# Optimization experiments

Measured on AMD Instinct MI355X. Metric: run time of the kernel, lower is better.

Reference implementation:

```python
import jax, jax.numpy as jnp
import numpy as np

N = 100000   # num_nodes
E = 1250000  # num_edges
IN = 64
HID = 64
OUT = 64
LN_EPS = 1e-5


def _gcn_conv(x, src, dst, W, b, n):
    # PyG GCNConv: add self-loops, symmetric deg^{-1/2} normalization, then linear.
    h = x @ W  # (N, out)
    deg = jax.ops.segment_sum(jnp.ones(src.shape[0], h.dtype), dst, num_segments=n) + 1.0  # +1 self-loop
    dinv = jax.lax.rsqrt(deg)
    norm = dinv[src] * dinv[dst]  # (E,)
    out = jax.ops.segment_sum(h[src] * norm[:, None], dst, num_segments=n)
    out = out + h * (dinv * dinv)[:, None]  # self-loop message
    return out + b


def _sage_conv(x, src, dst, Wl, bl, Wr, n):
    # PyG SAGEConv(aggr='mean'): lin_l(mean_{j in N(i)} x_j) + lin_r(x_i); bias only in lin_l.
    cnt = jax.ops.segment_sum(jnp.ones(src.shape[0], x.dtype), dst, num_segments=n)
    agg = jax.ops.segment_sum(x[src], dst, num_segments=n) / jnp.maximum(cnt, 1.0)[:, None]
    return agg @ Wl + bl + x @ Wr


def _layer_norm(x, g, b):
    mu = jnp.mean(x, axis=-1, keepdims=True)
    var = jnp.var(x, axis=-1, keepdims=True)
    return (x - mu) * jax.lax.rsqrt(var + LN_EPS) * g + b


def setup_inputs() -> dict:
    key = jax.random.key(0)
    ks = jax.random.split(key, 16)
    def w(k, shape):
        fan_in = shape[0]
        return (jax.random.normal(k, shape, jnp.float32) / np.sqrt(fan_in)).astype(jnp.float32)
    x = jax.random.normal(ks[0], (N, IN), jnp.float32)
    edge_index = jax.random.randint(ks[1], (2, E), 0, N, dtype=jnp.int64)
    return {
        "x": x,
        "edge_index": edge_index,
        "gcn_w1": w(ks[2], (IN, HID)), "gcn_b1": jnp.zeros((HID,), jnp.float32),
        "gcn_w2": w(ks[3], (HID, OUT)), "gcn_b2": jnp.zeros((OUT,), jnp.float32),
        "sage_wl1": w(ks[4], (IN, HID)), "sage_bl1": jnp.zeros((HID,), jnp.float32),
        "sage_wr1": w(ks[5], (IN, HID)),
        "sage_wl2": w(ks[6], (HID, OUT)), "sage_bl2": jnp.zeros((OUT,), jnp.float32),
        "sage_wr2": w(ks[7], (HID, OUT)),
        "gcn_ln_g": jnp.ones((OUT,), jnp.float32), "gcn_ln_b": jnp.zeros((OUT,), jnp.float32),
        "sage_ln_g": jnp.ones((OUT,), jnp.float32), "sage_ln_b": jnp.zeros((OUT,), jnp.float32),
        "proj_w": w(ks[8], (2 * OUT, OUT)), "proj_b": jnp.zeros((OUT,), jnp.float32),
    }


def reference(x, edge_index, gcn_w1, gcn_b1, gcn_w2, gcn_b2,
              sage_wl1, sage_bl1, sage_wr1, sage_wl2, sage_bl2, sage_wr2,
              gcn_ln_g, gcn_ln_b, sage_ln_g, sage_ln_b, proj_w, proj_b):
    src, dst = edge_index[0], edge_index[1]
    n = x.shape[0]
    # GCN branch (dropout p=0 / eval -> identity)
    g = jax.nn.relu(_gcn_conv(x, src, dst, gcn_w1, gcn_b1, n))
    g = _gcn_conv(g, src, dst, gcn_w2, gcn_b2, n)
    # SAGE branch
    s = jax.nn.relu(_sage_conv(x, src, dst, sage_wl1, sage_bl1, sage_wr1, n))
    s = _sage_conv(s, src, dst, sage_wl2, sage_bl2, sage_wr2, n)
    # Norm + projected-concat fusion
    g = _layer_norm(g, gcn_ln_g, gcn_ln_b)
    s = _layer_norm(s, sage_ln_g, sage_ln_b)
    cat = jnp.concatenate([g, s], axis=-1)  # (N, 2*OUT)
    return cat @ proj_w + proj_b
```

## Files before the change

kernel.cpp:

```cpp
#include <hip/hip_runtime.h>


#define SCAN_CHUNK 2048

typedef __attribute__((ext_vector_type(8))) short short8;
typedef __attribute__((ext_vector_type(4))) short short4v;
typedef __attribute__((ext_vector_type(4))) float floatx4;

__device__ __forceinline__ unsigned short f2bf(float f) {
    unsigned int u = __float_as_uint(f);
    unsigned int r = u + 0x7FFFu + ((u >> 16) & 1u);
    return (unsigned short)(r >> 16);
}
__device__ __forceinline__ float bf2f(unsigned short h) {
    return __uint_as_float(((unsigned int)h) << 16);
}

__device__ __forceinline__ unsigned lds_addr(const void* p) {
    return (unsigned)(unsigned long long)(__attribute__((address_space(3))) const char*)p;
}

__device__ __forceinline__ short8 cat44(short4v lo, short4v hi) {
    short8 r;
    r[0] = lo[0]; r[1] = lo[1]; r[2] = lo[2]; r[3] = lo[3];
    r[4] = hi[0]; r[5] = hi[1]; r[6] = hi[2]; r[7] = hi[3];
    return r;
}

template<int NF, int CTB>
__device__ __forceinline__ void tr_read4(unsigned a0, short8 bf[4]) {
    short4v l0, h0, l1, h1, l2, h2, l3, h3;
    asm volatile(
        "ds_read_b64_tr_b16 %0, %8 offset:%9\n\t"
        "ds_read_b64_tr_b16 %1, %8 offset:%10\n\t"
        "ds_read_b64_tr_b16 %2, %8 offset:%11\n\t"
        "ds_read_b64_tr_b16 %3, %8 offset:%12\n\t"
        "ds_read_b64_tr_b16 %4, %8 offset:%13\n\t"
        "ds_read_b64_tr_b16 %5, %8 offset:%14\n\t"
        "ds_read_b64_tr_b16 %6, %8 offset:%15\n\t"
        "ds_read_b64_tr_b16 %7, %8 offset:%16\n\t"
        "s_waitcnt lgkmcnt(0)"
        : "=&v"(l0), "=&v"(h0), "=&v"(l1), "=&v"(h1),
          "=&v"(l2), "=&v"(h2), "=&v"(l3), "=&v"(h3)
        : "v"(a0),
          "i"((0 * NF + CTB + 0) * 128), "i"((1 * NF + CTB + 0) * 128),
          "i"((0 * NF + CTB + 1) * 128), "i"((1 * NF + CTB + 1) * 128),
          "i"((0 * NF + CTB + 2) * 128), "i"((1 * NF + CTB + 2) * 128),
          "i"((0 * NF + CTB + 3) * 128), "i"((1 * NF + CTB + 3) * 128)
        : "memory");
    bf[0] = cat44(l0, h0);
    bf[1] = cat44(l1, h1);
    bf[2] = cat44(l2, h2);
    bf[3] = cat44(l3, h3);
}

__global__ void k_count(const int* __restrict__ ei, int E, int* __restrict__ cnt,
                        int* __restrict__ rank,
                        const float* __restrict__ x, unsigned short* __restrict__ xb,
                        int xtotal, int do_x) {
    int i = blockIdx.x * blockDim.x + threadIdx.x;
    int e = i * 4;
    if (e + 4 <= E) {
        int4 d = *(const int4*)&ei[E + e];
        int4 r;
        r.x = atomicAdd(&cnt[d.x], 1);
        r.y = atomicAdd(&cnt[d.y], 1);
        r.z = atomicAdd(&cnt[d.z], 1);
        r.w = atomicAdd(&cnt[d.w], 1);
        *(int4*)&rank[e] = r;
    } else if (e < E) {
        for (int j = e; j < E; ++j) rank[j] = atomicAdd(&cnt[ei[E + j]], 1);
    }
    if (do_x) {
        int xe = i * 8;
        if (xe + 8 <= xtotal) {
            float4 a = *(const float4*)&x[xe];
            float4 b = *(const float4*)&x[xe + 4];
            short8 o;
            o[0] = (short)f2bf(a.x); o[1] = (short)f2bf(a.y);
            o[2] = (short)f2bf(a.z); o[3] = (short)f2bf(a.w);
            o[4] = (short)f2bf(b.x); o[5] = (short)f2bf(b.y);
            o[6] = (short)f2bf(b.z); o[7] = (short)f2bf(b.w);
            *(short8*)&xb[xe] = o;
        } else if (xe < xtotal) {
            for (int j = xe; j < xtotal; ++j) xb[j] = f2bf(x[j]);
        }
    }
}

__global__ void k_scan_reduce(const int* __restrict__ cnt, int N, int* __restrict__ blockSums) {
    __shared__ int lds[256];
    int base = blockIdx.x * SCAN_CHUNK;
    int t = threadIdx.x;
    int s = 0;
    for (int j = 0; j < 8; ++j) {
        int idx = base + t * 8 + j;
        if (idx < N) s += cnt[idx] + 1;
    }
    lds[t] = s;
    __syncthreads();
    for (int d = 128; d > 0; d >>= 1) {
        if (t < d) lds[t] += lds[t + d];
        __syncthreads();
    }
    if (t == 0) blockSums[blockIdx.x] = lds[0];
}

__global__ void k_scan_spine(int* __restrict__ blockSums, int B) {
    if (threadIdx.x == 0 && blockIdx.x == 0) {
        int run = 0;
        for (int b = 0; b < B; ++b) { int v = blockSums[b]; blockSums[b] = run; run += v; }
    }
}

__global__ void k_scan_write(const int* __restrict__ cnt, int N,
                             const int* __restrict__ blockSums,
                             int* __restrict__ offs, float* __restrict__ dinv) {
    __shared__ int lds[256];
    int base = blockIdx.x * SCAN_CHUNK;
    int t = threadIdx.x;
    int v[8];
    int s = 0;
    for (int j = 0; j < 8; ++j) {
        int idx = base + t * 8 + j;
        v[j] = (idx < N) ? cnt[idx] : 0;
        s += (idx < N) ? v[j] + 1 : 0;
    }
    lds[t] = s;
    __syncthreads();
    for (int d = 1; d < 256; d <<= 1) {
        int x = (t >= d) ? lds[t - d] : 0;
        __syncthreads();
        lds[t] += x;
        __syncthreads();
    }
    int excl = (t == 0) ? 0 : lds[t - 1];
    int run = blockSums[blockIdx.x] + excl;
    for (int j = 0; j < 8; ++j) {
        int idx = base + t * 8 + j;
        if (idx < N) {
            offs[idx] = run;
            run += v[j] + 1;
            dinv[idx] = rsqrtf((float)v[j] + 1.0f);
            if (idx == N - 1) offs[N] = run;
        }
    }
}

__global__ void k_fill(const int* __restrict__ ei, int E, const int* __restrict__ offs,
                       const int* __restrict__ rank, const int* __restrict__ cnt,
                       const float* __restrict__ dinv,
                       int* __restrict__ csr, unsigned int* __restrict__ pk,
                       int use_pk, int N) {
    int i = blockIdx.x * blockDim.x + threadIdx.x;
    int e = i * 4;
    if (e + 4 <= E) {
        int4 s = *(const int4*)&ei[e];
        int4 d = *(const int4*)&ei[E + e];
        int4 r = *(const int4*)&rank[e];
        int p0 = offs[d.x] + r.x, p1 = offs[d.y] + r.y;
        int p2 = offs[d.z] + r.z, p3 = offs[d.w] + r.w;
        csr[p0] = s.x; csr[p1] = s.y; csr[p2] = s.z; csr[p3] = s.w;
        if (use_pk) {
            pk[p0] = ((unsigned)(d.x & 15) << 16) | f2bf(dinv[s.x] * dinv[d.x]);
            pk[p1] = ((unsigned)(d.y & 15) << 16) | f2bf(dinv[s.y] * dinv[d.y]);
            pk[p2] = ((unsigned)(d.z & 15) << 16) | f2bf(dinv[s.z] * dinv[d.z]);
            pk[p3] = ((unsigned)(d.w & 15) << 16) | f2bf(dinv[s.w] * dinv[d.w]);
        }
    } else if (e < E) {
        for (int j = e; j < E; ++j) {
            int dd = ei[E + j];
            int p = offs[dd] + rank[j];
            csr[p] = ei[j];
            if (use_pk) pk[p] = ((unsigned)(dd & 15) << 16) | f2bf(dinv[ei[j]] * dinv[dd]);
        }
    }
    if (use_pk && i < N) {
        int pos = offs[i] + cnt[i];
        float di = dinv[i];
        csr[pos] = i;
        pk[pos] = ((unsigned)(i & 15) << 16) | (1u << 20) | f2bf(di * di);
    }
}

template<int ROWSH>
__launch_bounds__(256)
__global__ void k_gatherM(const unsigned short* __restrict__ feat,
                          const int* __restrict__ csr,
                          const unsigned int* __restrict__ pk,
                          const int* __restrict__ offs, const int* __restrict__ cnt,
                          unsigned short* __restrict__ agg, int N) {
    constexpr int NF = ROWSH / 16;
    constexpr int LPR = ROWSH / 8;
    constexpr int EPP = 64 / LPR;
    constexpr int PASSES = 32 / EPP;

    __shared__ unsigned short sbuf[4][32 * ROWSH];

    const int lane = threadIdx.x & 63;
    const int wv = threadIdx.x >> 6;
    const int base = blockIdx.x * 64 + wv * 16;
    if (base >= N) return;

    const int q = lane >> 4;
    const int d16 = lane & 15;

    const int parity = lane & 1;
    const int ei_low = (lane >> 1) & 3;
    const int sf_sub = (lane >> 3) & (NF - 1);
    const int ei_high = (NF == 8) ? 0 : (lane >> 5);
    const int eid = ei_high * 4 + ei_low;
    const int sf = sf_sub * 16 + parity * 8;

    const int elo = offs[base];
    const int ehi = offs[min(base + 16, N)];
    const int emax = ehi - 1;
    const int nch = (ehi - elo + 31) >> 5;

    int cM0, cM1, cM2, cM3;
    unsigned pM0, pM1, pM2, pM3;
    {
        int i0 = elo + lane;
        int i1 = i0 + 64, i2 = i0 + 128, i3 = i0 + 192;
        cM0 = csr[i0 <= emax ? i0 : emax];
        cM1 = csr[i1 <= emax ? i1 : emax];
        cM2 = csr[i2 <= emax ? i2 : emax];
        cM3 = csr[i3 <= emax ? i3 : emax];
        unsigned t0 = pk[i0 <= emax ? i0 : emax];
        unsigned t1 = pk[i1 <= emax ? i1 : emax];
        unsigned t2 = pk[i2 <= emax ? i2 : emax];
        unsigned t3 = pk[i3 <= emax ? i3 : emax];
        pM0 = (i0 < ehi) ? t0 : 0x00100000u;
        pM1 = (i1 < ehi) ? t1 : 0x00100000u;
        pM2 = (i2 < ehi) ? t2 : 0x00100000u;
        pM3 = (i3 < ehi) ? t3 : 0x00100000u;
    }

    floatx4 accg[4], accs[4];
#pragma unroll
    for (int i = 0; i < 4; ++i) {
        accg[i] = floatx4{0.f, 0.f, 0.f, 0.f};
        accs[i] = floatx4{0.f, 0.f, 0.f, 0.f};
    }

    unsigned short* wb = &sbuf[wv][0];
    const unsigned a0 = lds_addr(wb) + (unsigned)(q * 2 * NF) * 128u + (unsigned)d16 * 8u;

    for (int c = 0; c < nch; ++c) {
        int cv; unsigned pv; int wofs;
        int rc = c >> 1;
        if (rc < 4) {
            wofs = (c & 1) << 5;
            cv = (rc == 0) ? cM0 : (rc == 1) ? cM1 : (rc == 2) ? cM2 : cM3;
            pv = (rc == 0) ? pM0 : (rc == 1) ? pM1 : (rc == 2) ? pM2 : pM3;
        } else {
            int idx = elo + (c << 5) + lane;
            int idc = idx <= emax ? idx : emax;
            cv = csr[idc];
            unsigned t = pk[idc];
            pv = (idx < ehi) ? t : 0x00100000u;
            wofs = 0;
        }

        short8 stg[PASSES];
#pragma unroll
        for (int p = 0; p < PASSES; ++p) {
            int src = __shfl(cv, wofs + p * EPP + eid, 64);
            stg[p] = *(const short8*)&feat[(size_t)src * ROWSH + sf];
        }

        short8 aG, aS;
#pragma unroll
        for (int j = 0; j < 8; ++j) {
            unsigned u = (unsigned)__shfl((int)pv, wofs + q * 8 + j, 64);
            unsigned hi = u >> 16;
            bool match = (int)(hi & 15u) == d16;
            aG[j] = match ? (short)(u & 0xFFFFu) : (short)0;
            aS[j] = (match && !(hi & 16u)) ? (short)0x3F80 : (short)0;
        }

#pragma unroll
        for (int p = 0; p < PASSES; ++p)
            *(short8*)&wb[p * 512 + lane * 8] = stg[p];
        asm volatile("s_waitcnt lgkmcnt(0)" ::: "memory");
        __builtin_amdgcn_sched_barrier(0);

        short8 bG[4];
        tr_read4<NF, 0>(a0, bG);
#pragma unroll
        for (int ct = 0; ct < 4; ++ct)
            accg[ct] = __builtin_amdgcn_mfma_f32_16x16x32_bf16(aG, bG[ct], accg[ct], 0, 0, 0);
        if constexpr (NF == 8) {
            short8 bS[4];
            tr_read4<NF, 4>(a0, bS);
#pragma unroll
            for (int ct = 0; ct < 4; ++ct)
                accs[ct] = __builtin_amdgcn_mfma_f32_16x16x32_bf16(aS, bS[ct], accs[ct], 0, 0, 0);
        } else {
#pragma unroll
            for (int ct = 0; ct < 4; ++ct)
                accs[ct] = __builtin_amdgcn_mfma_f32_16x16x32_bf16(aS, bG[ct], accs[ct], 0, 0, 0);
        }
    }

#pragma unroll
    for (int r = 0; r < 4; ++r) {
        int node = base + q * 4 + r;
        if (node < N) {
            float rn = 1.0f / fmaxf((float)cnt[node], 1.0f);
#pragma unroll
            for (int ct = 0; ct < 4; ++ct) {
                agg[(size_t)node * 128 + ct * 16 + d16]      = f2bf(accg[ct][r]);
                agg[(size_t)node * 128 + 64 + ct * 16 + d16] = f2bf(accs[ct][r] * rn);
            }
        }
    }
}

__device__ __forceinline__ void xor_reduce8(float4& a, float4& b) {
    a.x += __shfl_xor(a.x, 16, 64); a.y += __shfl_xor(a.y, 16, 64);
    a.z += __shfl_xor(a.z, 16, 64); a.w += __shfl_xor(a.w, 16, 64);
    b.x += __shfl_xor(b.x, 16, 64); b.y += __shfl_xor(b.y, 16, 64);
    b.z += __shfl_xor(b.z, 16, 64); b.w += __shfl_xor(b.w, 16, 64);
    a.x += __shfl_xor(a.x, 32, 64); a.y += __shfl_xor(a.y, 32, 64);
    a.z += __shfl_xor(a.z, 32, 64); a.w += __shfl_xor(a.w, 32, 64);
    b.x += __shfl_xor(b.x, 32, 64); b.y += __shfl_xor(b.y, 32, 64);
    b.z += __shfl_xor(b.z, 32, 64); b.w += __shfl_xor(b.w, 32, 64);
}

__device__ __forceinline__ float red16(float v) {
    v += __shfl_xor(v, 1, 64);
    v += __shfl_xor(v, 2, 64);
    v += __shfl_xor(v, 4, 64);
    v += __shfl_xor(v, 8, 64);
    return v;
}

__global__ void k_gather1_f32(const float* __restrict__ x, const int* __restrict__ csr,
                              const int* __restrict__ offs, const int* __restrict__ cnt,
                              const float* __restrict__ dinv,
                              unsigned short* __restrict__ agg, int N) {
    int lane = threadIdx.x & 63;
    int wave = threadIdx.x >> 6;
    int node = blockIdx.x * 4 + wave;
    if (node >= N) return;
    int c = lane & 15, grp = lane >> 4;

    int st = offs[node];
    int cn = cnt[node];
    float di = dinv[node];

    float4 aA = {0.f, 0.f, 0.f, 0.f}, aB = {0.f, 0.f, 0.f, 0.f};
    for (int e = 0; e < cn; e += 8) {
        int i0 = e + grp, i1 = e + 4 + grp;
        float m0 = (i0 < cn) ? 1.f : 0.f;
        float m1 = (i1 < cn) ? 1.f : 0.f;
        int s0 = csr[st + (i0 < cn ? i0 : cn - 1)];
        int s1 = csr[st + (i1 < cn ? i1 : cn - 1)];
        float w0 = m0 * dinv[s0];
        float w1 = m1 * dinv[s1];
        float4 v0 = *(const float4*)&x[(size_t)s0 * 64 + 4 * c];
        float4 v1 = *(const float4*)&x[(size_t)s1 * 64 + 4 * c];
        aA.x += w0 * v0.x + w1 * v1.x; aA.y += w0 * v0.y + w1 * v1.y;
        aA.z += w0 * v0.z + w1 * v1.z; aA.w += w0 * v0.w + w1 * v1.w;
        aB.x += m0 * v0.x + m1 * v1.x; aB.y += m0 * v0.y + m1 * v1.y;
        aB.z += m0 * v0.z + m1 * v1.z; aB.w += m0 * v0.w + m1 * v1.w;
    }
    xor_reduce8(aA, aB);

    if (grp == 0) {
        float4 sq = *(const float4*)&x[(size_t)node * 64 + 4 * c];
        float d2 = di * di;
        ushort4 o;
        o.x = f2bf(di * aA.x + d2 * sq.x); o.y = f2bf(di * aA.y + d2 * sq.y);
        o.z = f2bf(di * aA.z + d2 * sq.z); o.w = f2bf(di * aA.w + d2 * sq.w);
        *(ushort4*)&agg[(size_t)node * 128 + 4 * c] = o;
    } else if (grp == 1) {
        float rn = 1.0f / fmaxf((float)cn, 1.0f);
        ushort4 o;
        o.x = f2bf(aB.x * rn); o.y = f2bf(aB.y * rn);
        o.z = f2bf(aB.z * rn); o.w = f2bf(aB.w * rn);
        *(ushort4*)&agg[(size_t)node * 128 + 64 + 4 * c] = o;
    }
}

__global__ void k_gather2(const unsigned short* __restrict__ gs, const int* __restrict__ csr,
                          const int* __restrict__ offs, const int* __restrict__ cnt,
                          const float* __restrict__ dinv,
                          unsigned short* __restrict__ agg, int N) {
    int lane = threadIdx.x & 63;
    int wave = threadIdx.x >> 6;
    int node = blockIdx.x * 4 + wave;
    if (node >= N) return;
    int c = lane & 15, grp = lane >> 4;

    int st = offs[node];
    int cn = cnt[node];
    float di = dinv[node];

    float4 aC = {0.f, 0.f, 0.f, 0.f}, aD = {0.f, 0.f, 0.f, 0.f};
    for (int e = 0; e < cn; e += 8) {
        int i0 = e + grp, i1 = e + 4 + grp;
        float m0 = (i0 < cn) ? 1.f : 0.f;
        float m1 = (i1 < cn) ? 1.f : 0.f;
        int s0 = csr[st + (i0 < cn ? i0 : cn - 1)];
        int s1 = csr[st + (i1 < cn ? i1 : cn - 1)];
        float w0 = m0 * dinv[s0];
        float w1 = m1 * dinv[s1];
        const unsigned short* p0 = gs + (size_t)s0 * 128 + 4 * c;
        const unsigned short* p1 = gs + (size_t)s1 * 128 + 4 * c;
        ushort4 g0u = *(const ushort4*)p0;
        ushort4 g1u = *(const ushort4*)p1;
        ushort4 t0u = *(const ushort4*)(p0 + 64);
        ushort4 t1u = *(const ushort4*)(p1 + 64);
        aC.x += w0 * bf2f(g0u.x) + w1 * bf2f(g1u.x);
        aC.y += w0 * bf2f(g0u.y) + w1 * bf2f(g1u.y);
        aC.z += w0 * bf2f(g0u.z) + w1 * bf2f(g1u.z);
        aC.w += w0 * bf2f(g0u.w) + w1 * bf2f(g1u.w);
        aD.x += m0 * bf2f(t0u.x) + m1 * bf2f(t1u.x);
        aD.y += m0 * bf2f(t0u.y) + m1 * bf2f(t1u.y);
        aD.z += m0 * bf2f(t0u.z) + m1 * bf2f(t1u.z);
        aD.w += m0 * bf2f(t0u.w) + m1 * bf2f(t1u.w);
    }
    xor_reduce8(aC, aD);

    if (grp == 0) {
        ushort4 su = *(const ushort4*)&gs[(size_t)node * 128 + 4 * c];
        float d2 = di * di;
        ushort4 o;
        o.x = f2bf(di * aC.x + d2 * bf2f(su.x));
        o.y = f2bf(di * aC.y + d2 * bf2f(su.y));
        o.z = f2bf(di * aC.z + d2 * bf2f(su.z));
        o.w = f2bf(di * aC.w + d2 * bf2f(su.w));
        *(ushort4*)&agg[(size_t)node * 128 + 4 * c] = o;
    } else if (grp == 1) {
        float rn = 1.0f / fmaxf((float)cn, 1.0f);
        ushort4 o;
        o.x = f2bf(aD.x * rn); o.y = f2bf(aD.y * rn);
        o.z = f2bf(aD.z * rn); o.w = f2bf(aD.w * rn);
        *(ushort4*)&agg[(size_t)node * 128 + 64 + 4 * c] = o;
    }
}

__launch_bounds__(512, 1)
__global__ void k_gemm1(const unsigned short* __restrict__ agg,
                        const unsigned short* __restrict__ xb,
                        const float* __restrict__ xf, int use_xb,
                        const float* __restrict__ W1, const float* __restrict__ b1,
                        const float* __restrict__ Wl1, const float* __restrict__ bl1,
                        const float* __restrict__ Wr1,
                        unsigned short* __restrict__ buf1, int N) {
    alignas(16) __shared__ unsigned short sW[3][4096];
    int t = threadIdx.x;
    for (int i = t; i < 1536; i += 512) {
        int m = i >> 9;
        int rem = i & 511;
        int f = rem >> 6;
        int L = rem & 63;
        int kb = (f >> 2) * 32 + (L >> 4) * 8;
        int o = (f & 3) * 16 + (L & 15);
        const float* Wsrc = (m == 0) ? W1 : (m == 1) ? Wl1 : Wr1;
        unsigned short* dst = &sW[m][f * 512 + L * 8];
        #pragma unroll
        for (int j = 0; j < 8; ++j) dst[j] = f2bf(Wsrc[(kb + j) * 64 + o]);
    }
    __syncthreads();

    int lane = t & 63;
    int wave = t >> 6;
    int quad = lane >> 4;
    int n16 = lane & 15;
    int base = blockIdx.x * 128 + wave * 16;
    if (base >= N) return;

    int nm = base + n16;
    if (nm >= N) nm = N - 1;
    const unsigned short* ar = agg + (size_t)nm * 128;

    {
        short8 a0 = *(const short8*)(ar + quad * 8);
        short8 a1 = *(const short8*)(ar + 32 + quad * 8);
        floatx4 g0 = {0.f, 0.f, 0.f, 0.f}, g1 = g0, g2 = g0, g3 = g0;
        g0 = __builtin_amdgcn_mfma_f32_16x16x32_bf16(a0, *(const short8*)&sW[0][0 * 512 + lane * 8], g0, 0, 0, 0);
        g0 = __builtin_amdgcn_mfma_f32_16x16x32_bf16(a1, *(const short8*)&sW[0][4 * 512 + lane * 8], g0, 0, 0, 0);
        g1 = __builtin_amdgcn_mfma_f32_16x16x32_bf16(a0, *(const short8*)&sW[0][1 * 512 + lane * 8], g1, 0, 0, 0);
        g1 = __builtin_amdgcn_mfma_f32_16x16x32_bf16(a1, *(const short8*)&sW[0][5 * 512 + lane * 8], g1, 0, 0, 0);
        g2 = __builtin_amdgcn_mfma_f32_16x16x32_bf16(a0, *(const short8*)&sW[0][2 * 512 + lane * 8], g2, 0, 0, 0);
        g2 = __builtin_amdgcn_mfma_f32_16x16x32_bf16(a1, *(const short8*)&sW[0][6 * 512 + lane * 8], g2, 0, 0, 0);
        g3 = __builtin_amdgcn_mfma_f32_16x16x32_bf16(a0, *(const short8*)&sW[0][3 * 512 + lane * 8], g3, 0, 0, 0);
        g3 = __builtin_amdgcn_mfma_f32_16x16x32_bf16(a1, *(const short8*)&sW[0][7 * 512 + lane * 8], g3, 0, 0, 0);
        floatx4 gt[4] = {g0, g1, g2, g3};
        #pragma unroll
        for (int nt = 0; nt < 4; ++nt) {
            float bg = b1[nt * 16 + n16];
            #pragma unroll
            for (int r = 0; r < 4; ++r) {
                int node = base + quad * 4 + r;
                if (node < N)
                    buf1[(size_t)node * 128 + nt * 16 + n16] = f2bf(fmaxf(gt[nt][r] + bg, 0.f));
            }
        }
    }

    {
        short8 a0 = *(const short8*)(ar + 64 + quad * 8);
        short8 a1 = *(const short8*)(ar + 96 + quad * 8);
        short8 ax0, ax1;
        if (use_xb) {
            ax0 = *(const short8*)&xb[(size_t)nm * 64 + quad * 8];
            ax1 = *(const short8*)&xb[(size_t)nm * 64 + 32 + quad * 8];
        } else {
            float4 xq0 = *(const float4*)&xf[(size_t)nm * 64 + quad * 8];
            float4 xq1 = *(const float4*)&xf[(size_t)nm * 64 + quad * 8 + 4];
            float4 xq2 = *(const float4*)&xf[(size_t)nm * 64 + 32 + quad * 8];
            float4 xq3 = *(const float4*)&xf[(size_t)nm * 64 + 32 + quad * 8 + 4];
            ax0[0] = (short)f2bf(xq0.x); ax0[1] = (short)f2bf(xq0.y);
            ax0[2] = (short)f2bf(xq0.z); ax0[3] = (short)f2bf(xq0.w);
            ax0[4] = (short)f2bf(xq1.x); ax0[5] = (short)f2bf(xq1.y);
            ax0[6] = (short)f2bf(xq1.z); ax0[7] = (short)f2bf(xq1.w);
            ax1[0] = (short)f2bf(xq2.x); ax1[1] = (short)f2bf(xq2.y);
            ax1[2] = (short)f2bf(xq2.z); ax1[3] = (short)f2bf(xq2.w);
            ax1[4] = (short)f2bf(xq3.x); ax1[5] = (short)f2bf(xq3.y);
            ax1[6] = (short)f2bf(xq3.z); ax1[7] = (short)f2bf(xq3.w);
        }

        floatx4 s0 = {0.f, 0.f, 0.f, 0.f}, s1 = s0, s2 = s0, s3 = s0;
        s0 = __builtin_amdgcn_mfma_f32_16x16x32_bf16(a0, *(const short8*)&sW[1][0 * 512 + lane * 8], s0, 0, 0, 0);
        s0 = __builtin_amdgcn_mfma_f32_16x16x32_bf16(a1, *(const short8*)&sW[1][4 * 512 + lane * 8], s0, 0, 0, 0);
        s0 = __builtin_amdgcn_mfma_f32_16x16x32_bf16(ax0, *(const short8*)&sW[2][0 * 512 + lane * 8], s0, 0, 0, 0);
        s0 = __builtin_amdgcn_mfma_f32_16x16x32_bf16(ax1, *(const short8*)&sW[2][4 * 512 + lane * 8], s0, 0, 0, 0);
        s1 = __builtin_amdgcn_mfma_f32_16x16x32_bf16(a0, *(const short8*)&sW[1][1 * 512 + lane * 8], s1, 0, 0, 0);
        s1 = __builtin_amdgcn_mfma_f32_16x16x32_bf16(a1, *(const short8*)&sW[1][5 * 512 + lane * 8], s1, 0, 0, 0);
        s1 = __builtin_amdgcn_mfma_f32_16x16x32_bf16(ax0, *(const short8*)&sW[2][1 * 512 + lane * 8], s1, 0, 0, 0);
        s1 = __builtin_amdgcn_mfma_f32_16x16x32_bf16(ax1, *(const short8*)&sW[2][5 * 512 + lane * 8], s1, 0, 0, 0);
        s2 = __builtin_amdgcn_mfma_f32_16x16x32_bf16(a0, *(const short8*)&sW[1][2 * 512 + lane * 8], s2, 0, 0, 0);
        s2 = __builtin_amdgcn_mfma_f32_16x16x32_bf16(a1, *(const short8*)&sW[1][6 * 512 + lane * 8], s2, 0, 0, 0);
        s2 = __builtin_amdgcn_mfma_f32_16x16x32_bf16(ax0, *(const short8*)&sW[2][2 * 512 + lane * 8], s2, 0, 0, 0);
        s2 = __builtin_amdgcn_mfma_f32_16x16x32_bf16(ax1, *(const short8*)&sW[2][6 * 512 + lane * 8], s2, 0, 0, 0);
        s3 = __builtin_amdgcn_mfma_f32_16x16x32_bf16(a0, *(const short8*)&sW[1][3 * 512 + lane * 8], s3, 0, 0, 0);
        s3 = __builtin_amdgcn_mfma_f32_16x16x32_bf16(a1, *(const short8*)&sW[1][7 * 512 + lane * 8], s3, 0, 0, 0);
        s3 = __builtin_amdgcn_mfma_f32_16x16x32_bf16(ax0, *(const short8*)&sW[2][3 * 512 + lane * 8], s3, 0, 0, 0);
        s3 = __builtin_amdgcn_mfma_f32_16x16x32_bf16(ax1, *(const short8*)&sW[2][7 * 512 + lane * 8], s3, 0, 0, 0);
        floatx4 stl[4] = {s0, s1, s2, s3};
        #pragma unroll
        for (int nt = 0; nt < 4; ++nt) {
            float bs = bl1[nt * 16 + n16];
            #pragma unroll
            for (int r = 0; r < 4; ++r) {
                int node = base + quad * 4 + r;
                if (node < N)
                    buf1[(size_t)node * 128 + 64 + nt * 16 + n16] = f2bf(fmaxf(stl[nt][r] + bs, 0.f));
            }
        }
    }
}

__launch_bounds__(512, 1)
__global__ void k_gemm2(const unsigned short* __restrict__ agg,
                        const unsigned short* __restrict__ buf1,
                        const float* __restrict__ W2, const float* __restrict__ b2,
                        const float* __restrict__ Wl2, const float* __restrict__ bl2,
                        const float* __restrict__ Wr2,
                        const float* __restrict__ lngG, const float* __restrict__ lnbG,
                        const float* __restrict__ lngS, const float* __restrict__ lnbS,
                        const float* __restrict__ Pw, const float* __restrict__ Pb,
                        float* __restrict__ out, int N) {
    alignas(16) __shared__ unsigned short sW[3][4096];
    alignas(16) __shared__ unsigned short sP[8192];
    alignas(16) __shared__ unsigned short sT[8][16 * 132];
    int t = threadIdx.x;
    for (int i = t; i < 1536; i += 512) {
        int m = i >> 9;
        int rem = i & 511;
        int f = rem >> 6;
        int L = rem & 63;
        int kb = (f >> 2) * 32 + (L >> 4) * 8;
        int o = (f & 3) * 16 + (L & 15);
        const float* Wsrc = (m == 0) ? W2 : (m == 1) ? Wl2 : Wr2;
        unsigned short* dst = &sW[m][f * 512 + L * 8];
        #pragma unroll
        for (int j = 0; j < 8; ++j) dst[j] = f2bf(Wsrc[(kb + j) * 64 + o]);
    }
    for (int i = t; i < 1024; i += 512) {
        int f = i >> 6;
        int L = i & 63;
        int kb = (f >> 2) * 32 + (L >> 4) * 8;
        int o = (f & 3) * 16 + (L & 15);
        unsigned short* dst = &sP[f * 512 + L * 8];
        #pragma unroll
        for (int j = 0; j < 8; ++j) dst[j] = f2bf(Pw[(kb + j) * 64 + o]);
    }
    __syncthreads();

    int lane = t & 63;
    int wave = t >> 6;
    int quad = lane >> 4;
    int n16 = lane & 15;
    int base = blockIdx.x * 128 + wave * 16;
    if (base >= N) return;
    int nm = base + n16;
    if (nm >= N) nm = N - 1;
    const unsigned short* ar = agg + (size_t)nm * 128;
    const unsigned short* br = buf1 + (size_t)nm * 128;
    unsigned short* tw = &sT[wave][0];

    {
        short8 a0 = *(const short8*)(ar + quad * 8);
// ... 41 lines not shown
        c1 = __builtin_amdgcn_mfma_f32_16x16x32_bf16(a1, *(const short8*)&sW[1][5 * 512 + lane * 8], c1, 0, 0, 0);
        c1 = __builtin_amdgcn_mfma_f32_16x16x32_bf16(v0, *(const short8*)&sW[2][1 * 512 + lane * 8], c1, 0, 0, 0);
        c1 = __builtin_amdgcn_mfma_f32_16x16x32_bf16(v1, *(const short8*)&sW[2][5 * 512 + lane * 8], c1, 0, 0, 0);
        c2 = __builtin_amdgcn_mfma_f32_16x16x32_bf16(a0, *(const short8*)&sW[1][2 * 512 + lane * 8], c2, 0, 0, 0);
        c2 = __builtin_amdgcn_mfma_f32_16x16x32_bf16(a1, *(const short8*)&sW[1][6 * 512 + lane * 8], c2, 0, 0, 0);
        c2 = __builtin_amdgcn_mfma_f32_16x16x32_bf16(v0, *(const short8*)&sW[2][2 * 512 + lane * 8], c2, 0, 0, 0);
        c2 = __builtin_amdgcn_mfma_f32_16x16x32_bf16(v1, *(const short8*)&sW[2][6 * 512 + lane * 8], c2, 0, 0, 0);
        c3 = __builtin_amdgcn_mfma_f32_16x16x32_bf16(a0, *(const short8*)&sW[1][3 * 512 + lane * 8], c3, 0, 0, 0);
        c3 = __builtin_amdgcn_mfma_f32_16x16x32_bf16(a1, *(const short8*)&sW[1][7 * 512 + lane * 8], c3, 0, 0, 0);
        c3 = __builtin_amdgcn_mfma_f32_16x16x32_bf16(v0, *(const short8*)&sW[2][3 * 512 + lane * 8], c3, 0, 0, 0);
        c3 = __builtin_amdgcn_mfma_f32_16x16x32_bf16(v1, *(const short8*)&sW[2][7 * 512 + lane * 8], c3, 0, 0, 0);

        float bv0 = bl2[n16], bv1 = bl2[16 + n16], bv2 = bl2[32 + n16], bv3 = bl2[48 + n16];
        float gv0 = lngS[n16], gv1 = lngS[16 + n16], gv2 = lngS[32 + n16], gv3 = lngS[48 + n16];
        float ev0 = lnbS[n16], ev1 = lnbS[16 + n16], ev2 = lnbS[32 + n16], ev3 = lnbS[48 + n16];
        #pragma unroll
        for (int r = 0; r < 4; ++r) {
            float z0 = c0[r] + bv0, z1 = c1[r] + bv1, z2 = c2[r] + bv2, z3 = c3[r] + bv3;
            float s = red16(z0 + z1 + z2 + z3);
            float q = red16(z0 * z0 + z1 * z1 + z2 * z2 + z3 * z3);
            float mu = s * (1.0f / 64.0f);
            float var = fmaxf(q * (1.0f / 64.0f) - mu * mu, 0.0f);
            float rs = rsqrtf(var + 1e-5f);
            unsigned short* row = tw + (quad * 4 + r) * 132 + 64;
            row[n16]      = f2bf((z0 - mu) * rs * gv0 + ev0);
            row[16 + n16] = f2bf((z1 - mu) * rs * gv1 + ev1);
            row[32 + n16] = f2bf((z2 - mu) * rs * gv2 + ev2);
            row[48 + n16] = f2bf((z3 - mu) * rs * gv3 + ev3);
        }
    }

    floatx4 o0 = {0.f, 0.f, 0.f, 0.f}, o1 = o0, o2 = o0, o3 = o0;
    #pragma unroll
    for (int ks = 0; ks < 4; ++ks) {
        const unsigned short* ap = tw + n16 * 132 + ks * 32 + quad * 8;
        short4v lo = *(const short4v*)ap;
        short4v hi = *(const short4v*)(ap + 4);
        short8 af;
        af[0] = lo[0]; af[1] = lo[1]; af[2] = lo[2]; af[3] = lo[3];
        af[4] = hi[0]; af[5] = hi[1]; af[6] = hi[2]; af[7] = hi[3];
        o0 = __builtin_amdgcn_mfma_f32_16x16x32_bf16(af, *(const short8*)&sP[(ks * 4 + 0) * 512 + lane * 8], o0, 0, 0, 0);
        o1 = __builtin_amdgcn_mfma_f32_16x16x32_bf16(af, *(const short8*)&sP[(ks * 4 + 1) * 512 + lane * 8], o1, 0, 0, 0);
        o2 = __builtin_amdgcn_mfma_f32_16x16x32_bf16(af, *(const short8*)&sP[(ks * 4 + 2) * 512 + lane * 8], o2, 0, 0, 0);
        o3 = __builtin_amdgcn_mfma_f32_16x16x32_bf16(af, *(const short8*)&sP[(ks * 4 + 3) * 512 + lane * 8], o3, 0, 0, 0);
    }
    float p0 = Pb[n16], p1 = Pb[16 + n16], p2 = Pb[32 + n16], p3 = Pb[48 + n16];
    floatx4 ot[4] = {o0, o1, o2, o3};
    float pv[4] = {p0, p1, p2, p3};
    #pragma unroll
    for (int nt = 0; nt < 4; ++nt) {
        #pragma unroll
        for (int r = 0; r < 4; ++r) {
            int node = base + quad * 4 + r;
            if (node < N) out[(size_t)node * 64 + nt * 16 + n16] = ot[nt][r] + pv[nt];
        }
    }
}

extern "C" void kernel_launch(void* const* d_in, const int* in_sizes, int n_in,
                              void* d_out, int out_size, void* d_ws, size_t ws_size,
                              hipStream_t stream) {
    const float* x        = (const float*)d_in[0];
    const int*   ei       = (const int*)d_in[1];
    const float* gcn_w1   = (const float*)d_in[2];
    const float* gcn_b1   = (const float*)d_in[3];
    const float* gcn_w2   = (const float*)d_in[4];
    const float* gcn_b2   = (const float*)d_in[5];
    const float* sage_wl1 = (const float*)d_in[6];
    const float* sage_bl1 = (const float*)d_in[7];
    const float* sage_wr1 = (const float*)d_in[8];
    const float* sage_wl2 = (const float*)d_in[9];
    const float* sage_bl2 = (const float*)d_in[10];
    const float* sage_wr2 = (const float*)d_in[11];
    const float* gcn_ln_g = (const float*)d_in[12];
    const float* gcn_ln_b = (const float*)d_in[13];
    const float* sage_ln_g = (const float*)d_in[14];
    const float* sage_ln_b = (const float*)d_in[15];
    const float* proj_w   = (const float*)d_in[16];
    const float* proj_b   = (const float*)d_in[17];
    float* out = (float*)d_out;

    const int N = in_sizes[0] / 64;
    const int E = in_sizes[1] / 2;
    const int B = (N + SCAN_CHUNK - 1) / SCAN_CHUNK;

    char* w = (char*)d_ws;
    size_t off = 0;
    auto alloc = [&](size_t bytes) -> void* {
        void* p = w + off;
        off = (off + bytes + 255) & ~(size_t)255;
        return p;
    };
    int*            cnt       = (int*)alloc((size_t)N * 4);
    int*            offs      = (int*)alloc((size_t)(N + 1) * 4);
    float*          dinv      = (float*)alloc((size_t)N * 4);
    int*            blockSums = (int*)alloc((size_t)(B + 1) * 4);
    int*            csr       = (int*)alloc((size_t)(E + N + 64) * 4);
    unsigned short* agg       = (unsigned short*)alloc((size_t)N * 128 * 2);
    unsigned short* buf1      = (unsigned short*)alloc((size_t)N * 128 * 2);
    size_t off_nonew = off;
    unsigned int*   pk        = (unsigned int*)alloc((size_t)(E + N + 64) * 4);
    unsigned short* xb        = (unsigned short*)alloc((size_t)N * 64 * 2);
    int use_new = (off <= ws_size) ? 1 : 0;
    if (!use_new) off = off_nonew;
    int* rank = (int*)agg;
    (void)n_in; (void)out_size;

    hipMemsetAsync(cnt, 0, (size_t)N * 4, stream);

    int e4Blocks = ((E + 3) / 4 + 255) / 256;
    int x8Blocks = ((N * 64 + 7) / 8 + 255) / 256;
    int cntBlocks = use_new ? max(e4Blocks, x8Blocks) : e4Blocks;
    k_count<<<cntBlocks, 256, 0, stream>>>(ei, E, cnt, rank, x, xb, N * 64, use_new);
    k_scan_reduce<<<B, 256, 0, stream>>>(cnt, N, blockSums);
    k_scan_spine<<<1, 64, 0, stream>>>(blockSums, B);
    k_scan_write<<<B, 256, 0, stream>>>(cnt, N, blockSums, offs, dinv);
    k_fill<<<e4Blocks, 256, 0, stream>>>(ei, E, offs, rank, cnt, dinv, csr, pk, use_new, N);

    if (use_new) {
        k_gatherM<64><<<(N + 63) / 64, 256, 0, stream>>>(xb, csr, pk, offs, cnt, agg, N);
        k_gemm1<<<(N + 127) / 128, 512, 0, stream>>>(agg, xb, x, 1, gcn_w1, gcn_b1,
                                                     sage_wl1, sage_bl1, sage_wr1, buf1, N);
        k_gatherM<128><<<(N + 63) / 64, 256, 0, stream>>>(buf1, csr, pk, offs, cnt, agg, N);
    } else {
        k_gather1_f32<<<(N + 3) / 4, 256, 0, stream>>>(x, csr, offs, cnt, dinv, agg, N);
        k_gemm1<<<(N + 127) / 128, 512, 0, stream>>>(agg, xb, x, 0, gcn_w1, gcn_b1,
                                                     sage_wl1, sage_bl1, sage_wr1, buf1, N);
        k_gather2<<<(N + 3) / 4, 256, 0, stream>>>(buf1, csr, offs, cnt, dinv, agg, N);
    }
    k_gemm2<<<(N + 127) / 128, 512, 0, stream>>>(agg, buf1, gcn_w2, gcn_b2,
                                                 sage_wl2, sage_bl2, sage_wr2,
                                                 gcn_ln_g, gcn_ln_b, sage_ln_g, sage_ln_b,
                                                 proj_w, proj_b, out, N);
}
```

Measured before the change: 334.4 us.

## Build CSR by 16-node groups using LDS histograms instead of global atomics

Replaces the per-node global-atomic counting and rank-based fill with a two-level counting sort. Each of 256 blocks builds a shared-memory histogram over 16-node destination groups, followed by column sums, a group scan, per-block base offsets and an LDS-atomic scatter. Degrees, self-loop slots and normalisation weights are then derived per group in separate passes. The fallback f32 gather path is removed. The aim is to cut contended global atomics and the rank array traffic, at the cost of more kernel launches, a serial per-group loop over 256 blocks, and unordered edges within each group.

Result: no change. 333.2 us (-0.4%).

```diff
diff --git a/kernel.cpp b/kernel.cpp
--- a/kernel.cpp
+++ b/kernel.cpp
@@ -2,6 +2,8 @@
 
 
 #define SCAN_CHUNK 2048
+#define NB 256
+#define GMAX 8192
 
 typedef __attribute__((ext_vector_type(8))) short short8;
 typedef __attribute__((ext_vector_type(4))) short short4v;
@@ -54,48 +56,52 @@
     bf[3] = cat44(l3, h3);
 }
 
-__global__ void k_count(const int* __restrict__ ei, int E, int* __restrict__ cnt,
-                        int* __restrict__ rank,
-                        const float* __restrict__ x, unsigned short* __restrict__ xb,
-                        int xtotal, int do_x) {
-    int i = blockIdx.x * blockDim.x + threadIdx.x;
-    int e = i * 4;
-    if (e + 4 <= E) {
-        int4 d = *(const int4*)&ei[E + e];
-        int4 r;
-        r.x = atomicAdd(&cnt[d.x], 1);
-        r.y = atomicAdd(&cnt[d.y], 1);
-        r.z = atomicAdd(&cnt[d.z], 1);
-        r.w = atomicAdd(&cnt[d.w], 1);
-        *(int4*)&rank[e] = r;
-    } else if (e < E) {
-        for (int j = e; j < E; ++j) rank[j] = atomicAdd(&cnt[ei[E + j]], 1);
-    }
-    if (do_x) {
-        int xe = i * 8;
-        if (xe + 8 <= xtotal) {
-            float4 a = *(const float4*)&x[xe];
-            float4 b = *(const float4*)&x[xe + 4];
-            short8 o;
-            o[0] = (short)f2bf(a.x); o[1] = (short)f2bf(a.y);
-            o[2] = (short)f2bf(a.z); o[3] = (short)f2bf(a.w);
-            o[4] = (short)f2bf(b.x); o[5] = (short)f2bf(b.y);
-            o[6] = (short)f2bf(b.z); o[7] = (short)f2bf(b.w);
-            *(short8*)&xb[xe] = o;
-        } else if (xe < xtotal) {
-            for (int j = xe; j < xtotal; ++j) xb[j] = f2bf(x[j]);
-        }
-    }
-}
-
-__global__ void k_scan_reduce(const int* __restrict__ cnt, int N, int* __restrict__ blockSums) {
+__global__ void k_hist(const int* __restrict__ ei, int E, int G,
+                       unsigned* __restrict__ counts,
+                       const float* __restrict__ x, unsigned short* __restrict__ xb,
+                       int xtotal) {
+    __shared__ unsigned hist[GMAX];
+    int t = threadIdx.x, b = blockIdx.x;
+    for (int i = t; i < G; i += 256) hist[i] = 0;
+    __syncthreads();
+    int ec = (E + NB - 1) / NB;
+    int lo = b * ec, hi = min(lo + ec, E);
+    for (int idx = lo + t; idx < hi; idx += 256)
+        atomicAdd(&hist[ei[E + idx] >> 4], 1u);
+    __syncthreads();
+    for (int i = t; i < G; i += 256) counts[(size_t)b * G + i] = hist[i];
+    int nv = xtotal >> 3;
+    for (int v = b * 256 + t; v < nv; v += NB * 256) {
+        int e = v * 8;
+        float4 a = *(const float4*)&x[e];
+        float4 c = *(const float4*)&x[e + 4];
+        short8 o;
+        o[0] = (short)f2bf(a.x); o[1] = (short)f2bf(a.y);
+        o[2] = (short)f2bf(a.z); o[3] = (short)f2bf(a.w);
+        o[4] = (short)f2bf(c.x); o[5] = (short)f2bf(c.y);
+        o[6] = (short)f2bf(c.z); o[7] = (short)f2bf(c.w);
+        *(short8*)&xb[e] = o;
+    }
+}
+
+__global__ void k_colsum(const unsigned* __restrict__ counts, int G,
+                         int* __restrict__ cnt16) {
+    int g = blockIdx.x * 256 + threadIdx.x;
+    if (g < G) {
+        int tot = 0;
+        for (int b = 0; b < NB; ++b) tot += (int)counts[(size_t)b * G + g];
+        cnt16[g] = tot;
+    }
+}
+
+__global__ void k_gr(const int* __restrict__ cnt16, int G, int* __restrict__ blockSums) {
     __shared__ int lds[256];
     int base = blockIdx.x * SCAN_CHUNK;
     int t = threadIdx.x;
     int s = 0;
     for (int j = 0; j < 8; ++j) {
         int idx = base + t * 8 + j;
-        if (idx < N) s += cnt[idx] + 1;
+        if (idx < G) s += cnt16[idx] + 16;
     }
     lds[t] = s;
     __syncthreads();
@@ -113,9 +119,8 @@
     }
 }
 
-__global__ void k_scan_write(const int* __restrict__ cnt, int N,
-                             const int* __restrict__ blockSums,
-                             int* __restrict__ offs, float* __restrict__ dinv) {
+__global__ void k_gw(const int* __restrict__ cnt16, int G,
+                     const int* __restrict__ blockSums, int* __restrict__ offs16) {
     __shared__ int lds[256];
     int base = blockIdx.x * SCAN_CHUNK;
     int t = threadIdx.x;
@@ -123,8 +128,8 @@
     int s = 0;
     for (int j = 0; j < 8; ++j) {
         int idx = base + t * 8 + j;
-        v[j] = (idx < N) ? cnt[idx] : 0;
-        s += (idx < N) ? v[j] + 1 : 0;
+        v[j] = (idx < G) ? cnt16[idx] : 0;
+        s += (idx < G) ? v[j] + 16 : 0;
     }
     lds[t] = s;
     __syncthreads();
@@ -138,48 +143,94 @@
     int run = blockSums[blockIdx.x] + excl;
     for (int j = 0; j < 8; ++j) {
         int idx = base + t * 8 + j;
-        if (idx < N) {
-            offs[idx] = run;
-            run += v[j] + 1;
-            dinv[idx] = rsqrtf((float)v[j] + 1.0f);
-            if (idx == N - 1) offs[N] = run;
-        }
-    }
-}
-
-__global__ void k_fill(const int* __restrict__ ei, int E, const int* __restrict__ offs,
-                       const int* __restrict__ rank, const int* __restrict__ cnt,
-                       const float* __restrict__ dinv,
-                       int* __restrict__ csr, unsigned int* __restrict__ pk,
-                       int use_pk, int N) {
-    int i = blockIdx.x * blockDim.x + threadIdx.x;
-    int e = i * 4;
-    if (e + 4 <= E) {
-        int4 s = *(const int4*)&ei[e];
-        int4 d = *(const int4*)&ei[E + e];
-        int4 r = *(const int4*)&rank[e];
-        int p0 = offs[d.x] + r.x, p1 = offs[d.y] + r.y;
-        int p2 = offs[d.z] + r.z, p3 = offs[d.w] + r.w;
-        csr[p0] = s.x; csr[p1] = s.y; csr[p2] = s.z; csr[p3] = s.w;
-        if (use_pk) {
-            pk[p0] = ((unsigned)(d.x & 15) << 16) | f2bf(dinv[s.x] * dinv[d.x]);
-            pk[p1] = ((unsigned)(d.y & 15) << 16) | f2bf(dinv[s.y] * dinv[d.y]);
-            pk[p2] = ((unsigned)(d.z & 15) << 16) | f2bf(dinv[s.z] * dinv[d.z]);
-            pk[p3] = ((unsigned)(d.w & 15) << 16) | f2bf(dinv[s.w] * dinv[d.w]);
-        }
-    } else if (e < E) {
-        for (int j = e; j < E; ++j) {
-            int dd = ei[E + j];
-            int p = offs[dd] + rank[j];
-            csr[p] = ei[j];
-            if (use_pk) pk[p] = ((unsigned)(dd & 15) << 16) | f2bf(dinv[ei[j]] * dinv[dd]);
-        }
-    }
-    if (use_pk && i < N) {
-        int pos = offs[i] + cnt[i];
-        float di = dinv[i];
-        csr[pos] = i;
-        pk[pos] = ((unsigned)(i & 15) << 16) | (1u << 20) | f2bf(di * di);
+        if (idx < G) {
+            offs16[idx] = run;
+            run += v[j] + 16;
+            if (idx == G - 1) offs16[G] = run;
+        }
+    }
+}
+
+__global__ void k_bases(unsigned* __restrict__ counts, int G,
+                        const int* __restrict__ offs16) {
+    int g = blockIdx.x * 256 + threadIdx.x;
+    if (g >= G) return;
+    unsigned run = (unsigned)offs16[g];
+    for (int b = 0; b < NB; ++b) {
+        unsigned v = counts[(size_t)b * G + g];
+        counts[(size_t)b * G + g] = run;
+        run += v;
+    }
+}
+
+__global__ void k_scatter(const int* __restrict__ ei, int E, int G,
+                          const unsigned* __restrict__ counts,
+                          int* __restrict__ csr, unsigned* __restrict__ pk) {
+    __shared__ unsigned cur[GMAX];
+    int t = threadIdx.x, b = blockIdx.x;
+    for (int i = t; i < G; i += 256) cur[i] = counts[(size_t)b * G + i];
+    __syncthreads();
+    int ec = (E + NB - 1) / NB;
+    int lo = b * ec, hi = min(lo + ec, E);
+    for (int idx = lo + t; idx < hi; idx += 256) {
+        int s = ei[idx];
+        int d = ei[E + idx];
+        unsigned pos = atomicAdd(&cur[d >> 4], 1u);
+        csr[pos] = s;
+        pk[pos] = (unsigned)(d & 15) << 16;
+    }
+}
+
+__global__ void k_degself(const int* __restrict__ offs16, int G, int N,
+                          int* __restrict__ cnt, float* __restrict__ dinv,
+                          int* __restrict__ csr, unsigned* __restrict__ pk) {
+    __shared__ int wcnt[4][16];
+    int lane = threadIdx.x & 63;
+    int wv = threadIdx.x >> 6;
+    int g = blockIdx.x * 4 + wv;
+    bool act = (g < G);
+    if (lane < 16) wcnt[wv][lane] = 0;
+    __syncthreads();
+    if (act) {
+        int lo = offs16[g];
+        int rh = offs16[g + 1] - 16;
+        for (int idx = lo + lane; idx < rh; idx += 64) {
+            int d15 = (int)((pk[idx] >> 16) & 15u);
+            atomicAdd(&wcnt[wv][d15], 1);
+        }
+    }
+    __syncthreads();
+    if (act && lane < 16) {
+        int rh = offs16[g + 1] - 16;
+        int deg = wcnt[wv][lane];
+        int node = g * 16 + lane;
+        int slot = rh + lane;
+        if (node < N) {
+            cnt[node] = deg;
+            float di = rsqrtf((float)deg + 1.0f);
+            dinv[node] = di;
+            csr[slot] = node;
+            pk[slot] = ((unsigned)lane << 16) | (1u << 20) | f2bf(di * di);
+        } else {
+            csr[slot] = 0;
+            pk[slot] = ((unsigned)lane << 16) | (1u << 20);
+        }
+    }
+}
+
+__global__ void k_weights(const int* __restrict__ csr, const int* __restrict__ offs16,
+                          int G, int N, const float* __restrict__ dinv,
+                          unsigned* __restrict__ pk) {
+    int lane = threadIdx.x & 63;
+    int g = blockIdx.x * 4 + (threadIdx.x >> 6);
+    if (g >= G) return;
+    int lo = offs16[g];
+    int rh = offs16[g + 1] - 16;
+    for (int idx = lo + lane; idx < rh; idx += 64) {
+        unsigned u = pk[idx];
+        int s = csr[idx];
+        int dst = g * 16 + (int)((u >> 16) & 15u);
+        pk[idx] = u | f2bf(dinv[s] * dinv[dst]);
     }
 }
 
@@ -188,7 +239,7 @@
 __global__ void k_gatherM(const unsigned short* __restrict__ feat,
                           const int* __restrict__ csr,
                           const unsigned int* __restrict__ pk,
-                          const int* __restrict__ offs, const int* __restrict__ cnt,
+                          const int* __restrict__ offs16, const int* __restrict__ cnt,
                           unsigned short* __restrict__ agg, int N) {
     constexpr int NF = ROWSH / 16;
     constexpr int LPR = ROWSH / 8;
@@ -212,8 +263,9 @@
     const int eid = ei_high * 4 + ei_low;
     const int sf = sf_sub * 16 + parity * 8;
 
-    const int elo = offs[base];
-    const int ehi = offs[min(base + 16, N)];
+    const int grp = base >> 4;
+    const int elo = offs16[grp];
+    const int ehi = offs16[grp + 1];
     const int emax = ehi - 1;
     const int nch = (ehi - elo + 31) >> 5;
 
@@ -317,17 +369,6 @@
     }
 }
 
-__device__ __forceinline__ void xor_reduce8(float4& a, float4& b) {
-    a.x += __shfl_xor(a.x, 16, 64); a.y += __shfl_xor(a.y, 16, 64);
-    a.z += __shfl_xor(a.z, 16, 64); a.w += __shfl_xor(a.w, 16, 64);
-    b.x += __shfl_xor(b.x, 16, 64); b.y += __shfl_xor(b.y, 16, 64);
-    b.z += __shfl_xor(b.z, 16, 64); b.w += __shfl_xor(b.w, 16, 64);
-    a.x += __shfl_xor(a.x, 32, 64); a.y += __shfl_xor(a.y, 32, 64);
-    a.z += __shfl_xor(a.z, 32, 64); a.w += __shfl_xor(a.w, 32, 64);
-    b.x += __shfl_xor(b.x, 32, 64); b.y += __shfl_xor(b.y, 32, 64);
-    b.z += __shfl_xor(b.z, 32, 64); b.w += __shfl_xor(b.w, 32, 64);
-}
-
 __device__ __forceinline__ float red16(float v) {
     v += __shfl_xor(v, 1, 64);
     v += __shfl_xor(v, 2, 64);
@@ -336,116 +377,9 @@
     return v;
 }
 
-__global__ void k_gather1_f32(const float* __restrict__ x, const int* __restrict__ csr,
-                              const int* __restrict__ offs, const int* __restrict__ cnt,
-                              const float* __restrict__ dinv,
-                              unsigned short* __restrict__ agg, int N) {
-    int lane = threadIdx.x & 63;
-    int wave = threadIdx.x >> 6;
-    int node = blockIdx.x * 4 + wave;
-    if (node >= N) return;
-    int c = lane & 15, grp = lane >> 4;
-
-    int st = offs[node];
-    int cn = cnt[node];
-    float di = dinv[node];
-
-    float4 aA = {0.f, 0.f, 0.f, 0.f}, aB = {0.f, 0.f, 0.f, 0.f};
-    for (int e = 0; e < cn; e += 8) {
-        int i0 = e + grp, i1 = e + 4 + grp;
-        float m0 = (i0 < cn) ? 1.f : 0.f;
-        float m1 = (i1 < cn) ? 1.f : 0.f;
-        int s0 = csr[st + (i0 < cn ? i0 : cn - 1)];
-        int s1 = csr[st + (i1 < cn ? i1 : cn - 1)];
-        float w0 = m0 * dinv[s0];
-        float w1 = m1 * dinv[s1];
-        float4 v0 = *(const float4*)&x[(size_t)s0 * 64 + 4 * c];
-        float4 v1 = *(const float4*)&x[(size_t)s1 * 64 + 4 * c];
-        aA.x += w0 * v0.x + w1 * v1.x; aA.y += w0 * v0.y + w1 * v1.y;
-        aA.z += w0 * v0.z + w1 * v1.z; aA.w += w0 * v0.w + w1 * v1.w;
-        aB.x += m0 * v0.x + m1 * v1.x; aB.y += m0 * v0.y + m1 * v1.y;
-        aB.z += m0 * v0.z + m1 * v1.z; aB.w += m0 * v0.w + m1 * v1.w;
-    }
-    xor_reduce8(aA, aB);
-
-    if (grp == 0) {
-        float4 sq = *(const float4*)&x[(size_t)node * 64 + 4 * c];
-        float d2 = di * di;
-        ushort4 o;
-        o.x = f2bf(di * aA.x + d2 * sq.x); o.y = f2bf(di * aA.y + d2 * sq.y);
-        o.z = f2bf(di * aA.z + d2 * sq.z); o.w = f2bf(di * aA.w + d2 * sq.w);
-        *(ushort4*)&agg[(size_t)node * 128 + 4 * c] = o;
-    } else if (grp == 1) {
-        float rn = 1.0f / fmaxf((float)cn, 1.0f);
-        ushort4 o;
-        o.x = f2bf(aB.x * rn); o.y = f2bf(aB.y * rn);
-        o.z = f2bf(aB.z * rn); o.w = f2bf(aB.w * rn);
-        *(ushort4*)&agg[(size_t)node * 128 + 64 + 4 * c] = o;
-    }
-}
-
-__global__ void k_gather2(const unsigned short* __restrict__ gs, const int* __restrict__ csr,
-                          const int* __restrict__ offs, const int* __restrict__ cnt,
-                          const float* __restrict__ dinv,
-                          unsigned short* __restrict__ agg, int N) {
-    int lane = threadIdx.x & 63;
-    int wave = threadIdx.x >> 6;
-    int node = blockIdx.x * 4 + wave;
-    if (node >= N) return;
-    int c = lane & 15, grp = lane >> 4;
-
-    int st = offs[node];
-    int cn = cnt[node];
-    float di = dinv[node];
-
-    float4 aC = {0.f, 0.f, 0.f, 0.f}, aD = {0.f, 0.f, 0.f, 0.f};
-    for (int e = 0; e < cn; e += 8) {
-        int i0 = e + grp, i1 = e + 4 + grp;
-        float m0 = (i0 < cn) ? 1.f : 0.f;
-        float m1 = (i1 < cn) ? 1.f : 0.f;
-        int s0 = csr[st + (i0 < cn ? i0 : cn - 1)];
-        int s1 = csr[st + (i1 < cn ? i1 : cn - 1)];
-        float w0 = m0 * dinv[s0];
-        float w1 = m1 * dinv[s1];
-        const unsigned short* p0 = gs + (size_t)s0 * 128 + 4 * c;
-        const unsigned short* p1 = gs + (size_t)s1 * 128 + 4 * c;
-        ushort4 g0u = *(const ushort4*)p0;
-        ushort4 g1u = *(const ushort4*)p1;
-        ushort4 t0u = *(const ushort4*)(p0 + 64);
-        ushort4 t1u = *(const ushort4*)(p1 + 64);
-        aC.x += w0 * bf2f(g0u.x) + w1 * bf2f(g1u.x);
-        aC.y += w0 * bf2f(g0u.y) + w1 * bf2f(g1u.y);
-        aC.z += w0 * bf2f(g0u.z) + w1 * bf2f(g1u.z);
-        aC.w += w0 * bf2f(g0u.w) + w1 * bf2f(g1u.w);
-        aD.x += m0 * bf2f(t0u.x) + m1 * bf2f(t1u.x);
-        aD.y += m0 * bf2f(t0u.y) + m1 * bf2f(t1u.y);
-        aD.z += m0 * bf2f(t0u.z) + m1 * bf2f(t1u.z);
-        aD.w += m0 * bf2f(t0u.w) + m1 * bf2f(t1u.w);
-    }
-    xor_reduce8(aC, aD);
-
-    if (grp == 0) {
-        ushort4 su = *(const ushort4*)&gs[(size_t)node * 128 + 4 * c];
-        float d2 = di * di;
-        ushort4 o;
-        o.x = f2bf(di * aC.x + d2 * bf2f(su.x));
-        o.y = f2bf(di * aC.y + d2 * bf2f(su.y));
-        o.z = f2bf(di * aC.z + d2 * bf2f(su.z));
-        o.w = f2bf(di * aC.w + d2 * bf2f(su.w));
-        *(ushort4*)&agg[(size_t)node * 128 + 4 * c] = o;
-    } else if (grp == 1) {
-        float rn = 1.0f / fmaxf((float)cn, 1.0f);
-        ushort4 o;
-        o.x = f2bf(aD.x * rn); o.y = f2bf(aD.y * rn);
-        o.z = f2bf(aD.z * rn); o.w = f2bf(aD.w * rn);
-        *(ushort4*)&agg[(size_t)node * 128 + 64 + 4 * c] = o;
-    }
-}
-
 __launch_bounds__(512, 1)
 __global__ void k_gemm1(const unsigned short* __restrict__ agg,
                         const unsigned short* __restrict__ xb,
-                        const float* __restrict__ xf, int use_xb,
                         const float* __restrict__ W1, const float* __restrict__ b1,
                         const float* __restrict__ Wl1, const float* __restrict__ bl1,
                         const float* __restrict__ Wr1,
@@ -505,24 +439,8 @@
     {
         short8 a0 = *(const short8*)(ar + 64 + quad * 8);
         short8 a1 = *(const short8*)(ar + 96 + quad * 8);
-        short8 ax0, ax1;
-        if (use_xb) {
-            ax0 = *(const short8*)&xb[(size_t)nm * 64 + quad * 8];
-            ax1 = *(const short8*)&xb[(size_t)nm * 64 + 32 + quad * 8];
-        } else {
-            float4 xq0 = *(const float4*)&xf[(size_t)nm * 64 + quad * 8];
-            float4 xq1 = *(const float4*)&xf[(size_t)nm * 64 + quad * 8 + 4];
-            float4 xq2 = *(const float4*)&xf[(size_t)nm * 64 + 32 + quad * 8];
-            float4 xq3 = *(const float4*)&xf[(size_t)nm * 64 + 32 + quad * 8 + 4];
-            ax0[0] = (short)f2bf(xq0.x); ax0[1] = (short)f2bf(xq0.y);
-            ax0[2] = (short)f2bf(xq0.z); ax0[3] = (short)f2bf(xq0.w);
-            ax0[4] = (short)f2bf(xq1.x); ax0[5] = (short)f2bf(xq1.y);
-            ax0[6] = (short)f2bf(xq1.z); ax0[7] = (short)f2bf(xq1.w);
-            ax1[0] = (short)f2bf(xq2.x); ax1[1] = (short)f2bf(xq2.y);
-            ax1[2] = (short)f2bf(xq2.z); ax1[3] = (short)f2bf(xq2.w);
-            ax1[4] = (short)f2bf(xq3.x); ax1[5] = (short)f2bf(xq3.y);
-            ax1[6] = (short)f2bf(xq3.z); ax1[7] = (short)f2bf(xq3.w);
-        }
+        short8 ax0 = *(const short8*)&xb[(size_t)nm * 64 + quad * 8];
+        short8 ax1 = *(const short8*)&xb[(size_t)nm * 64 + 32 + quad * 8];
 
         floatx4 s0 = {0.f, 0.f, 0.f, 0.f}, s1 = s0, s2 = s0, s3 = s0;
         s0 = __builtin_amdgcn_mfma_f32_16x16x32_bf16(a0, *(const short8*)&sW[1][0 * 512 + lane * 8], s0, 0, 0, 0);
@@ -730,7 +648,8 @@
 
     const int N = in_sizes[0] / 64;
     const int E = in_sizes[1] / 2;
-    const int B = (N + SCAN_CHUNK - 1) / SCAN_CHUNK;
+    const int G = (N + 15) / 16;
+    const int Bg = (G + SCAN_CHUNK - 1) / SCAN_CHUNK;
 
     char* w = (char*)d_ws;
     size_t off = 0;
@@ -740,42 +659,32 @@
         return p;
     };
     int*            cnt       = (int*)alloc((size_t)N * 4);
-    int*            offs      = (int*)alloc((size_t)(N + 1) * 4);
+    int*            offs16    = (int*)alloc((size_t)(G + 1) * 4);
     float*          dinv      = (float*)alloc((size_t)N * 4);
-    int*            blockSums = (int*)alloc((size_t)(B + 1) * 4);
-    int*            csr       = (int*)alloc((size_t)(E + N + 64) * 4);
+    int*            blockSums = (int*)alloc((size_t)(Bg + 1) * 4);
+    int*            cnt16     = (int*)alloc((size_t)G * 4);
+    int*            csr       = (int*)alloc((size_t)(E + 16 * G + 64) * 4);
+    unsigned int*   pk        = (unsigned int*)alloc((size_t)(E + 16 * G + 64) * 4);
+    unsigned int*   counts    = (unsigned int*)alloc((size_t)NB * G * 4);
     unsigned short* agg       = (unsigned short*)alloc((size_t)N * 128 * 2);
     unsigned short* buf1      = (unsigned short*)alloc((size_t)N * 128 * 2);
-    size_t off_nonew = off;
-    unsigned int*   pk        = (unsigned int*)alloc((size_t)(E + N + 64) * 4);
     unsigned short* xb        = (unsigned short*)alloc((size_t)N * 64 * 2);
-    int use_new = (off <= ws_size) ? 1 : 0;
-    if (!use_new) off = off_nonew;
-    int* rank = (int*)agg;
-    (void)n_in; (void)out_size;
-
-    hipMemsetAsync(cnt, 0, (size_t)N * 4, stream);
-
-    int e4Blocks = ((E + 3) / 4 + 255) / 256;
-    int x8Blocks = ((N * 64 + 7) / 8 + 255) / 256;
-    int cntBlocks = use_new ? max(e4Blocks, x8Blocks) : e4Blocks;
-    k_count<<<cntBlocks, 256, 0, stream>>>(ei, E, cnt, rank, x, xb, N * 64, use_new);
-    k_scan_reduce<<<B, 256, 0, stream>>>(cnt, N, blockSums);
-    k_scan_spine<<<1, 64, 0, stream>>>(blockSums, B);
-    k_scan_write<<<B, 256, 0, stream>>>(cnt, N, blockSums, offs, dinv);
-    k_fill<<<e4Blocks, 256, 0, stream>>>(ei, E, offs, rank, cnt, dinv, csr, pk, use_new, N);
-
-    if (use_new) {
-        k_gatherM<64><<<(N + 63) / 64, 256, 0, stream>>>(xb, csr, pk, offs, cnt, agg, N);
-        k_gemm1<<<(N + 127) / 128, 512, 0, stream>>>(agg, xb, x, 1, gcn_w1, gcn_b1,
-                                                     sage_wl1, sage_bl1, sage_wr1, buf1, N);
-        k_gatherM<128><<<(N + 63) / 64, 256, 0, stream>>>(buf1, csr, pk, offs, cnt, agg, N);
-    } else {
-        k_gather1_f32<<<(N + 3) / 4, 256, 0, stream>>>(x, csr, offs, cnt, dinv, agg, N);
-        k_gemm1<<<(N + 127) / 128, 512, 0, stream>>>(agg, xb, x, 0, gcn_w1, gcn_b1,
-                                                     sage_wl1, sage_bl1, sage_wr1, buf1, N);
-        k_gather2<<<(N + 3) / 4, 256, 0, stream>>>(buf1, csr, offs, cnt, dinv, agg, N);
-    }
+    (void)n_in; (void)out_size; (void)ws_size;
+
+    k_hist<<<NB, 256, 0, stream>>>(ei, E, G, counts, x, xb, N * 64);
+    k_colsum<<<(G + 255) / 256, 256, 0, stream>>>(counts, G, cnt16);
+    k_gr<<<Bg, 256, 0, stream>>>(cnt16, G, blockSums);
+    k_scan_spine<<<1, 64, 0, stream>>>(blockSums, Bg);
+    k_gw<<<Bg, 256, 0, stream>>>(cnt16, G, blockSums, offs16);
+    k_bases<<<(G + 255) / 256, 256, 0, stream>>>(counts, G, offs16);
+    k_scatter<<<NB, 256, 0, stream>>>(ei, E, G, counts, csr, pk);
+    k_degself<<<(G + 3) / 4, 256, 0, stream>>>(offs16, G, N, cnt, dinv, csr, pk);
+    k_weights<<<(G + 3) / 4, 256, 0, stream>>>(csr, offs16, G, N, dinv, pk);
+
+    k_gatherM<64><<<(N + 63) / 64, 256, 0, stream>>>(xb, csr, pk, offs16, cnt, agg, N);
+    k_gemm1<<<(N + 127) / 128, 512, 0, stream>>>(agg, xb, gcn_w1, gcn_b1,
+                                                 sage_wl1, sage_bl1, sage_wr1, buf1, N);
+    k_gatherM<128><<<(N + 63) / 64, 256, 0, stream>>>(buf1, csr, pk, offs16, cnt, agg, N);
     k_gemm2<<<(N + 127) / 128, 512, 0, stream>>>(agg, buf1, gcn_w2, gcn_b2,
                                                  sage_wl2, sage_bl2, sage_wr2,
                                                  gcn_ln_g, gcn_ln_b, sage_ln_g, sage_ln_b,
```
